# Kernel optimization log

Measured on AMD Instinct MI355X. Metric: run time of the kernel, lower is better.

## Reference

```python
import jax, jax.numpy as jnp
import numpy as np

B, S, H = 32, 2048, 1024
UNITS = 1024


def setup_inputs() -> dict:
    key = jax.random.key(0)
    ks = jax.random.split(key, 8)
    scale_h = 1.0 / np.sqrt(H)
    scale_u = 1.0 / np.sqrt(UNITS)
    return {
        "query": jax.random.normal(ks[0], (B, H), dtype=jnp.float32),
        "values": jax.random.normal(ks[1], (B, S, H), dtype=jnp.float32),
        "W1": jax.random.normal(ks[2], (H, UNITS), dtype=jnp.float32) * scale_h,
        "b1": jnp.zeros((UNITS,), dtype=jnp.float32),
        "W2": jax.random.normal(ks[3], (H, UNITS), dtype=jnp.float32) * scale_h,
        "b2": jnp.zeros((UNITS,), dtype=jnp.float32),
        "V": jax.random.normal(ks[4], (UNITS, 1), dtype=jnp.float32) * scale_u,
        "bv": jnp.zeros((1,), dtype=jnp.float32),
    }


def reference(query, values, W1, b1, W2, b2, V, bv):
    # proj_v: [B, S, units]; proj_q: [B, 1, units] (query expanded on time axis)
    proj_v = jnp.einsum("bsh,hu->bsu", values, W1) + b1
    proj_q = (query @ W2 + b2)[:, None, :]
    # score: [B, S, 1]
    score = jnp.tanh(proj_v + proj_q) @ V + bv
    attention_weights = jax.nn.softmax(score, axis=1)  # softmax over seq axis
    context_vector = jnp.sum(attention_weights * values, axis=1)  # [B, H]
    return context_vector, attention_weights
```

## Files before the change

### kernel.cpp

```cpp
#include <hip/hip_runtime.h>

#define H 1024
#define UNITS 1024
#define BATCH 32
#define SEQ 2048
#define M_TOT (BATCH * SEQ)

typedef __attribute__((ext_vector_type(8))) short bf16x8;
typedef __attribute__((ext_vector_type(8))) unsigned short u16x8;
typedef __attribute__((ext_vector_type(4))) float f32x4;

__device__ __forceinline__ unsigned short f2bf(float f) {
  union { float f; unsigned u; } x; x.f = f;
  unsigned r = x.u + 0x7FFFu + ((x.u >> 16) & 1u);
  return (unsigned short)(r >> 16);
}
__device__ __forceinline__ float bf2f(unsigned short h) {
  union { unsigned u; float f; } x; x.u = (unsigned)h << 16;
  return x.f;
}

__device__ __forceinline__ void gll16(const unsigned short* g, unsigned short* l) {
  __builtin_amdgcn_global_load_lds(
      (const __attribute__((address_space(1))) void*)g,
      (__attribute__((address_space(3))) void*)l, 16, 0, 0);
}

__global__ void k_cast(const float* __restrict__ in, unsigned short* __restrict__ out) {
  size_t i = ((size_t)blockIdx.x * 256 + threadIdx.x) * 8;
  float4 v0 = *reinterpret_cast<const float4*>(in + i);
  float4 v1 = *reinterpret_cast<const float4*>(in + i + 4);
  union { unsigned short h[8]; u16x8 v; } p;
  p.h[0] = f2bf(v0.x); p.h[1] = f2bf(v0.y); p.h[2] = f2bf(v0.z); p.h[3] = f2bf(v0.w);
  p.h[4] = f2bf(v1.x); p.h[5] = f2bf(v1.y); p.h[6] = f2bf(v1.z); p.h[7] = f2bf(v1.w);
  *reinterpret_cast<u16x8*>(out + i) = p.v;
}

__global__ void k_transpose_w1(const float* __restrict__ W1, unsigned short* __restrict__ W1T) {
  __shared__ float tile[32][33];
  int bx = blockIdx.x, by = blockIdx.y;
  int tx = threadIdx.x, ty = threadIdx.y;
#pragma unroll
  for (int i = 0; i < 4; ++i)
    tile[ty + i * 8][tx] = W1[(by * 32 + ty + i * 8) * UNITS + bx * 32 + tx];
  __syncthreads();
#pragma unroll
  for (int i = 0; i < 4; ++i)
    W1T[(bx * 32 + ty + i * 8) * H + by * 32 + tx] = f2bf(tile[tx][ty + i * 8]);
}

__global__ void k_projq(const float* __restrict__ query, const float* __restrict__ W2,
                        const float* __restrict__ b2, float* __restrict__ projq) {
  __shared__ float q[H];
  int b = blockIdx.x;
  int u = blockIdx.y * 256 + threadIdx.x;
  for (int i = threadIdx.x; i < H; i += 256) q[i] = query[b * H + i];
  __syncthreads();
  float acc = 0.f;
#pragma unroll 8
  for (int k = 0; k < H; ++k) acc = fmaf(q[k], W2[k * UNITS + u], acc);
  projq[b * UNITS + u] = acc + b2[u];
}

#define BM 256
#define BN 256
#define NT 16

__global__ __launch_bounds__(512, 2) void k_score3(
    const unsigned short* __restrict__ Vb,
    const unsigned short* __restrict__ W1T,
    const float* __restrict__ b1,
    const float* __restrict__ projq,
    const float* __restrict__ V,
    float* __restrict__ scores)
{
  __shared__ unsigned short As[2][256][64];
  __shared__ unsigned short Bs[2][256][64];

  const int tid = threadIdx.x;
  const int lane = tid & 63;
  const int wave = tid >> 6;
  const int wm = wave >> 2;
  const int wn = wave & 3;
  const int li = lane & 15, hi = lane >> 4;
  const int lx = li & 7;

  const int g = blockIdx.x;
  const int xcd = g & 7;
  const int local = g >> 3;
  const int n_t = local & 3;
  const int m_t = xcd + ((local >> 2) << 3);
  const int m0 = m_t * BM;
  const int n0 = n_t * BN;

  const int crow = lane >> 3;
  const int scol = ((lane & 7) ^ crow) << 3;

  auto STAGE_A = [&](int bf, int kt) {
#pragma unroll
    for (int q = 0; q < 4; ++q) {
      int r = wave * 32 + q * 8;
      gll16(&Vb[(size_t)(m0 + r + crow) * H + kt * 64 + scol], &As[bf][r][0]);
    }
  };
  auto STAGE_B = [&](int bf, int kt) {
#pragma unroll
    for (int q = 0; q < 4; ++q) {
      int r = wave * 32 + q * 8;
      gll16(&W1T[(size_t)(n0 + r + crow) * H + kt * 64 + scol], &Bs[bf][r][0]);
    }
  };

  f32x4 acc[8][4] = {};

  STAGE_A(0, 0);
  STAGE_B(0, 0);

#pragma unroll 2
  for (int c = 0; c < NT; ++c) {
    const int buf = c & 1, nbuf = buf ^ 1;
    const int cn = (c < NT - 1) ? c + 1 : NT - 1;

    asm volatile("s_waitcnt vmcnt(0)" ::: "memory");
    __builtin_amdgcn_s_barrier();

    bf16x8 a[8], b0, b1v;

    STAGE_A(nbuf, cn);
#pragma unroll
    for (int i = 0; i < 8; ++i)
      a[i] = *reinterpret_cast<const bf16x8*>(
          &As[buf][wm * 128 + i * 16 + li][(hi ^ lx) << 3]);
    b0  = *reinterpret_cast<const bf16x8*>(&Bs[buf][wn * 64 +  0 + li][(hi ^ lx) << 3]);
    b1v = *reinterpret_cast<const bf16x8*>(&Bs[buf][wn * 64 + 16 + li][(hi ^ lx) << 3]);
    __builtin_amdgcn_s_setprio(1);
#pragma unroll
    for (int i = 0; i < 8; ++i) {
      acc[i][0] = __builtin_amdgcn_mfma_f32_16x16x32_bf16(a[i], b0, acc[i][0], 0, 0, 0);
      acc[i][1] = __builtin_amdgcn_mfma_f32_16x16x32_bf16(a[i], b1v, acc[i][1], 0, 0, 0);
    }
    __builtin_amdgcn_s_setprio(0);

    STAGE_B(nbuf, cn);
    b0  = *reinterpret_cast<const bf16x8*>(&Bs[buf][wn * 64 + 32 + li][(hi ^ lx) << 3]);
    b1v = *reinterpret_cast<const bf16x8*>(&Bs[buf][wn * 64 + 48 + li][(hi ^ lx) << 3]);
    __builtin_amdgcn_s_setprio(1);
#pragma unroll
    for (int i = 0; i < 8; ++i) {
      acc[i][2] = __builtin_amdgcn_mfma_f32_16x16x32_bf16(a[i], b0, acc[i][2], 0, 0, 0);
      acc[i][3] = __builtin_amdgcn_mfma_f32_16x16x32_bf16(a[i], b1v, acc[i][3], 0, 0, 0);
    }
    __builtin_amdgcn_s_setprio(0);

#pragma unroll
    for (int i = 0; i < 8; ++i)
      a[i] = *reinterpret_cast<const bf16x8*>(
          &As[buf][wm * 128 + i * 16 + li][((4 + hi) ^ lx) << 3]);
    b0  = *reinterpret_cast<const bf16x8*>(&Bs[buf][wn * 64 +  0 + li][((4 + hi) ^ lx) << 3]);
    b1v = *reinterpret_cast<const bf16x8*>(&Bs[buf][wn * 64 + 16 + li][((4 + hi) ^ lx) << 3]);
    __builtin_amdgcn_s_setprio(1);
#pragma unroll
    for (int i = 0; i < 8; ++i) {
      acc[i][0] = __builtin_amdgcn_mfma_f32_16x16x32_bf16(a[i], b0, acc[i][0], 0, 0, 0);
      acc[i][1] = __builtin_amdgcn_mfma_f32_16x16x32_bf16(a[i], b1v, acc[i][1], 0, 0, 0);
    }
    __builtin_amdgcn_s_setprio(0);

    b0  = *reinterpret_cast<const bf16x8*>(&Bs[buf][wn * 64 + 32 + li][((4 + hi) ^ lx) << 3]);
    b1v = *reinterpret_cast<const bf16x8*>(&Bs[buf][wn * 64 + 48 + li][((4 + hi) ^ lx) << 3]);
    __builtin_amdgcn_s_setprio(1);
#pragma unroll
    for (int i = 0; i < 8; ++i) {
      acc[i][2] = __builtin_amdgcn_mfma_f32_16x16x32_bf16(a[i], b0, acc[i][2], 0, 0, 0);
      acc[i][3] = __builtin_amdgcn_mfma_f32_16x16x32_bf16(a[i], b1v, acc[i][3], 0, 0, 0);
    }
    __builtin_amdgcn_s_setprio(0);
  }

  const int b = m0 >> 11;
  float bias[4], vv[4];
#pragma unroll
  for (int j = 0; j < 4; ++j) {
    int u = n0 + wn * 64 + j * 16 + li;
    bias[j] = b1[u] + projq[b * UNITS + u];
    vv[j] = V[u];
  }
#pragma unroll
  for (int mi = 0; mi < 8; ++mi) {
#pragma unroll
    for (int r = 0; r < 4; ++r) {
      float s = 0.f;
#pragma unroll
      for (int j = 0; j < 4; ++j) {
        float x = acc[mi][j][r] + bias[j];
        float e = __expf(2.f * x);
        s += (1.f - 2.f / (e + 1.f)) * vv[j];
      }
      s += __shfl_xor(s, 1);
      s += __shfl_xor(s, 2);
      s += __shfl_xor(s, 4);
      s += __shfl_xor(s, 8);
      if (li == 0) {
        int row = m0 + wm * 128 + mi * 16 + hi * 4 + r;
        atomicAdd(&scores[row], s);
      }
    }
  }
}

#define FBM 128
#define FBN 128
#define FBK 64
#define LDK 72
__global__ __launch_bounds__(256) void k_score_f32(
    const float* __restrict__ values, const unsigned short* __restrict__ W1T,
    const float* __restrict__ b1, const float* __restrict__ projq,
    const float* __restrict__ V, float* __restrict__ scores)
{
  __shared__ unsigned short Asf[FBM][LDK];
  __shared__ unsigned short Bsf[FBN][LDK];
  const int tid = threadIdx.x;
  const int lane = tid & 63;
  const int wave = tid >> 6;
  const int wm = wave >> 1, wn = wave & 1;
  const int li = lane & 15, hi = lane >> 4;
  const int n0 = blockIdx.x * FBN;
  const int m0 = blockIdx.y * FBM;
  f32x4 acc[4][4] = {};
  for (int k0 = 0; k0 < H; k0 += FBK) {
    __syncthreads();
#pragma unroll
    for (int q = 0; q < 8; ++q) {
      int idx = q * 256 + tid;
      int row = idx >> 4;
      int kc = (idx & 15) << 2;
      float4 v = *reinterpret_cast<const float4*>(&values[(size_t)(m0 + row) * H + k0 + kc]);
      union { unsigned short h[4]; unsigned long long u64; } p;
      p.h[0] = f2bf(v.x); p.h[1] = f2bf(v.y); p.h[2] = f2bf(v.z); p.h[3] = f2bf(v.w);
      *reinterpret_cast<unsigned long long*>(&Asf[row][kc]) = p.u64;
    }
#pragma unroll
    for (int q = 0; q < 4; ++q) {
      int idx = q * 256 + tid;
      int row = idx >> 3;
      int kc = (idx & 7) << 3;
      *reinterpret_cast<u16x8*>(&Bsf[row][kc]) =
          *reinterpret_cast<const u16x8*>(&W1T[(size_t)(n0 + row) * H + k0 + kc]);
    }
    __syncthreads();
#pragma unroll
    for (int ks = 0; ks < 2; ++ks) {
      const int kofs = ks * 32 + 8 * hi;
      bf16x8 a[4], bb[4];
#pragma unroll
      for (int i = 0; i < 4; ++i)
        a[i] = *reinterpret_cast<const bf16x8*>(&Asf[wm * 64 + i * 16 + li][kofs]);
#pragma unroll
      for (int i = 0; i < 4; ++i)
        bb[i] = *reinterpret_cast<const bf16x8*>(&Bsf[wn * 64 + i * 16 + li][kofs]);
#pragma unroll
      for (int mi = 0; mi < 4; ++mi)
#pragma unroll
        for (int ni = 0; ni < 4; ++ni)
          acc[mi][ni] = __builtin_amdgcn_mfma_f32_16x16x32_bf16(a[mi], bb[ni], acc[mi][ni], 0, 0, 0);
    }
  }
  const int b = m0 >> 11;
  float bias[4], vv[4];
#pragma unroll
  for (int ni = 0; ni < 4; ++ni) {
    int u = n0 + wn * 64 + ni * 16 + li;
    bias[ni] = b1[u] + projq[b * UNITS + u];
    vv[ni] = V[u];
  }
#pragma unroll
  for (int mi = 0; mi < 4; ++mi) {
#pragma unroll
    for (int r = 0; r < 4; ++r) {
      float s = 0.f;
#pragma unroll
      for (int ni = 0; ni < 4; ++ni) {
        float x = acc[mi][ni][r] + bias[ni];
        float e = __expf(2.f * x);
        s += (1.f - 2.f / (e + 1.f)) * vv[ni];
      }
      s += __shfl_xor(s, 1);
      s += __shfl_xor(s, 2);
      s += __shfl_xor(s, 4);
      s += __shfl_xor(s, 8);
      if (li == 0) atomicAdd(&scores[m0 + wm * 64 + mi * 16 + hi * 4 + r], s);
    }
  }
}

__global__ void k_softmax(const float* __restrict__ scores, float* __restrict__ wts) {
  __shared__ float red[8];
  int b = blockIdx.x;
  int t = threadIdx.x;
  float v[8];
  float mx = -3.4e38f;
#pragma unroll
  for (int i = 0; i < 8; ++i) {
    v[i] = scores[b * SEQ + i * 256 + t];
    mx = fmaxf(mx, v[i]);
  }
#pragma unroll
  for (int o = 1; o < 64; o <<= 1) mx = fmaxf(mx, __shfl_xor(mx, o));
  if ((t & 63) == 0) red[t >> 6] = mx;
  __syncthreads();
  mx = fmaxf(fmaxf(red[0], red[1]), fmaxf(red[2], red[3]));
  float sum = 0.f;
#pragma unroll
  for (int i = 0; i < 8; ++i) { v[i] = __expf(v[i] - mx); sum += v[i]; }
#pragma unroll
  for (int o = 1; o < 64; o <<= 1) sum += __shfl_xor(sum, o);
  if ((t & 63) == 0) red[4 + (t >> 6)] = sum;
  __syncthreads();
  float inv = 1.f / (red[4] + red[5] + red[6] + red[7]);
#pragma unroll
  for (int i = 0; i < 8; ++i) wts[b * SEQ + i * 256 + t] = v[i] * inv;
}

__global__ void k_context_bf(const unsigned short* __restrict__ Vb,
                             const float* __restrict__ wts, float* __restrict__ ctx) {
  int b = blockIdx.x, sc = blockIdx.y;
  int h4 = threadIdx.x * 4;
  const unsigned short* vb = Vb + (size_t)b * SEQ * H;
  float a0 = 0, a1 = 0, a2 = 0, a3 = 0;
  int s0 = sc * 128;
#pragma unroll 4
  for (int s = s0; s < s0 + 128; ++s) {
    float w = wts[b * SEQ + s];
    ushort4 v = *reinterpret_cast<const ushort4*>(&vb[(size_t)s * H + h4]);
    a0 = fmaf(w, bf2f(v.x), a0);
    a1 = fmaf(w, bf2f(v.y), a1);
    a2 = fmaf(w, bf2f(v.z), a2);
    a3 = fmaf(w, bf2f(v.w), a3);
  }
  atomicAdd(&ctx[b * H + h4 + 0], a0);
  atomicAdd(&ctx[b * H + h4 + 1], a1);
  atomicAdd(&ctx[b * H + h4 + 2], a2);
  atomicAdd(&ctx[b * H + h4 + 3], a3);
}

__global__ void k_context(const float* __restrict__ values, const float* __restrict__ wts,
                          float* __restrict__ ctx) {
  int b = blockIdx.x, hc = blockIdx.y, sc = blockIdx.z;
  int h = hc * 256 + threadIdx.x;
  const float* vb = values + (size_t)b * SEQ * H;
  float acc = 0.f;
  int s0 = sc * 128;
#pragma unroll 4
  for (int s = s0; s < s0 + 128; ++s)
    acc = fmaf(wts[b * SEQ + s], vb[(size_t)s * H + h], acc);
  atomicAdd(&ctx[b * H + h], acc);
}

extern "C" void kernel_launch(void* const* d_in, const int* in_sizes, int n_in,
                              void* d_out, int out_size, void* d_ws, size_t ws_size,
                              hipStream_t stream) {
  (void)in_sizes; (void)n_in; (void)out_size;
  const float* query  = (const float*)d_in[0];
  const float* values = (const float*)d_in[1];
  const float* W1     = (const float*)d_in[2];
  const float* b1     = (const float*)d_in[3];
  const float* W2     = (const float*)d_in[4];
  const float* b2     = (const float*)d_in[5];
  const float* V      = (const float*)d_in[6];

  float* out = (float*)d_out;
  float* ctx = out;
  float* wts = out + BATCH * H;

  const size_t vb_bytes = (size_t)M_TOT * H * 2;
  const size_t need = vb_bytes + (2u << 20) + (256u << 10) + (128u << 10);

  if (ws_size >= need) {
    char* ws = (char*)d_ws;
    unsigned short* Vb  = (unsigned short*)ws;
    unsigned short* W1T = (unsigned short*)(ws + vb_bytes);
    float* scores = (float*)(ws + vb_bytes + (2u << 20));
    float* projq  = (float*)(ws + vb_bytes + (2u << 20) + (256u << 10));

    hipMemsetAsync(scores, 0, M_TOT * sizeof(float), stream);
    hipMemsetAsync(ctx, 0, BATCH * H * sizeof(float), stream);

    k_cast<<<(M_TOT * H / 8) / 256, 256, 0, stream>>>(values, Vb);
    k_transpose_w1<<<dim3(32, 32), dim3(32, 8), 0, stream>>>(W1, W1T);
    k_projq<<<dim3(32, 4), 256, 0, stream>>>(query, W2, b2, projq);
    k_score3<<<(M_TOT / BM) * (UNITS / BN), 512, 0, stream>>>(Vb, W1T, b1, projq, V, scores);
    k_softmax<<<BATCH, 256, 0, stream>>>(scores, wts);
    k_context_bf<<<dim3(BATCH, 16), 256, 0, stream>>>(Vb, wts, ctx);
  } else {
    char* ws = (char*)d_ws;
    unsigned short* W1T = (unsigned short*)ws;
    float* scores = (float*)(ws + (2u << 20));
    float* projq  = (float*)(ws + (2u << 20) + (256u << 10));

    hipMemsetAsync(scores, 0, M_TOT * sizeof(float), stream);
    hipMemsetAsync(ctx, 0, BATCH * H * sizeof(float), stream);

    k_transpose_w1<<<dim3(32, 32), dim3(32, 8), 0, stream>>>(W1, W1T);
    k_projq<<<dim3(32, 4), 256, 0, stream>>>(query, W2, b2, projq);
    k_score_f32<<<dim3(UNITS / FBN, M_TOT / FBM), 256, 0, stream>>>(values, W1T, b1, projq, V, scores);
    k_softmax<<<BATCH, 256, 0, stream>>>(scores, wts);
    k_context<<<dim3(BATCH, H / 256, 16), 256, 0, stream>>>(values, wts, ctx);
  }
}
```

Baseline: 341.1 us.

## Deepen GEMM K-pipeline to four stages with K=32 tiles and repacked LDS layout

Switches the score GEMM main loop from a 2-buffer K=64 pipeline to a 4-buffer K=32 pipeline. Three tiles are prefetched ahead, and the wait is relaxed to vmcnt(8) so global loads stay in flight across iterations. The LDS layout packs two 32-wide rows per 64-short line with a new XOR swizzle, and all LDS reads are issued before the next stage's async loads. The goal is to hide global-load latency better, at the cost of twice as many barriers per K and a new swizzle whose correctness and bank-conflict behaviour have to hold.

After: 328.2 us. -3.8%, faster.

```diff
diff --git a/kernel.cpp b/kernel.cpp
--- a/kernel.cpp
+++ b/kernel.cpp
@@ -64,7 +64,7 @@
 
 #define BM 256
 #define BN 256
-#define NT 16
+#define NKT 32
 
 __global__ __launch_bounds__(512, 2) void k_score3(
     const unsigned short* __restrict__ Vb,
@@ -74,8 +74,8 @@
     const float* __restrict__ V,
     float* __restrict__ scores)
 {
-  __shared__ unsigned short As[2][256][64];
-  __shared__ unsigned short Bs[2][256][64];
+  __shared__ unsigned short As[4][128][64];
+  __shared__ unsigned short Bs[4][128][64];
 
   const int tid = threadIdx.x;
   const int lane = tid & 63;
@@ -83,7 +83,8 @@
   const int wm = wave >> 2;
   const int wn = wave & 3;
   const int li = lane & 15, hi = lane >> 4;
-  const int lx = li & 7;
+  const int lr2 = li >> 1;
+  const int pcol = (((((li & 1) << 2) + hi) ^ lr2) & 7) << 3;
 
   const int g = blockIdx.x;
   const int xcd = g & 7;
@@ -93,87 +94,58 @@
   const int m0 = m_t * BM;
   const int n0 = n_t * BN;
 
-  const int crow = lane >> 3;
-  const int scol = ((lane & 7) ^ crow) << 3;
+  const int sL = (lane & 7) ^ (lane >> 3);
+  const int srow = 2 * (lane >> 3) + (sL >> 2);
+  const int scol = (sL & 3) << 3;
 
   auto STAGE_A = [&](int bf, int kt) {
 #pragma unroll
-    for (int q = 0; q < 4; ++q) {
-      int r = wave * 32 + q * 8;
-      gll16(&Vb[(size_t)(m0 + r + crow) * H + kt * 64 + scol], &As[bf][r][0]);
+    for (int q = 0; q < 2; ++q) {
+      int mb = wave * 32 + q * 16;
+      gll16(&Vb[(size_t)(m0 + mb + srow) * H + kt * 32 + scol],
+            &As[bf][wave * 16 + q * 8][0]);
     }
   };
   auto STAGE_B = [&](int bf, int kt) {
 #pragma unroll
-    for (int q = 0; q < 4; ++q) {
-      int r = wave * 32 + q * 8;
-      gll16(&W1T[(size_t)(n0 + r + crow) * H + kt * 64 + scol], &Bs[bf][r][0]);
+    for (int q = 0; q < 2; ++q) {
+      int mb = wave * 32 + q * 16;
+      gll16(&W1T[(size_t)(n0 + mb + srow) * H + kt * 32 + scol],
+            &Bs[bf][wave * 16 + q * 8][0]);
     }
   };
 
   f32x4 acc[8][4] = {};
 
-  STAGE_A(0, 0);
-  STAGE_B(0, 0);
-
-#pragma unroll 2
-  for (int c = 0; c < NT; ++c) {
-    const int buf = c & 1, nbuf = buf ^ 1;
-    const int cn = (c < NT - 1) ? c + 1 : NT - 1;
-
-    asm volatile("s_waitcnt vmcnt(0)" ::: "memory");
+  STAGE_A(0, 0); STAGE_B(0, 0);
+  STAGE_A(1, 1); STAGE_B(1, 1);
+  STAGE_A(2, 2); STAGE_B(2, 2);
+
+#pragma unroll 4
+  for (int c = 0; c < NKT; ++c) {
+    const int buf = c & 3;
+    const int nbuf = (c + 3) & 3;
+    const int cn = (c < NKT - 3) ? c + 3 : NKT - 1;
+
+    asm volatile("s_waitcnt vmcnt(8)" ::: "memory");
     __builtin_amdgcn_s_barrier();
 
-    bf16x8 a[8], b0, b1v;
-
+    bf16x8 a[8], b[4];
+#pragma unroll
+    for (int i = 0; i < 8; ++i)
+      a[i] = *reinterpret_cast<const bf16x8*>(&As[buf][wm * 64 + i * 8 + lr2][pcol]);
     STAGE_A(nbuf, cn);
 #pragma unroll
+    for (int j = 0; j < 4; ++j)
+      b[j] = *reinterpret_cast<const bf16x8*>(&Bs[buf][wn * 32 + j * 8 + lr2][pcol]);
+    STAGE_B(nbuf, cn);
+
+    __builtin_amdgcn_s_setprio(1);
+#pragma unroll
     for (int i = 0; i < 8; ++i)
-      a[i] = *reinterpret_cast<const bf16x8*>(
-          &As[buf][wm * 128 + i * 16 + li][(hi ^ lx) << 3]);
-    b0  = *reinterpret_cast<const bf16x8*>(&Bs[buf][wn * 64 +  0 + li][(hi ^ lx) << 3]);
-    b1v = *reinterpret_cast<const bf16x8*>(&Bs[buf][wn * 64 + 16 + li][(hi ^ lx) << 3]);
-    __builtin_amdgcn_s_setprio(1);
-#pragma unroll
-    for (int i = 0; i < 8; ++i) {
-      acc[i][0] = __builtin_amdgcn_mfma_f32_16x16x32_bf16(a[i], b0, acc[i][0], 0, 0, 0);
-      acc[i][1] = __builtin_amdgcn_mfma_f32_16x16x32_bf16(a[i], b1v, acc[i][1], 0, 0, 0);
-    }
-    __builtin_amdgcn_s_setprio(0);
-
-    STAGE_B(nbuf, cn);
-    b0  = *reinterpret_cast<const bf16x8*>(&Bs[buf][wn * 64 + 32 + li][(hi ^ lx) << 3]);
-    b1v = *reinterpret_cast<const bf16x8*>(&Bs[buf][wn * 64 + 48 + li][(hi ^ lx) << 3]);
-    __builtin_amdgcn_s_setprio(1);
-#pragma unroll
-    for (int i = 0; i < 8; ++i) {
-      acc[i][2] = __builtin_amdgcn_mfma_f32_16x16x32_bf16(a[i], b0, acc[i][2], 0, 0, 0);
-      acc[i][3] = __builtin_amdgcn_mfma_f32_16x16x32_bf16(a[i], b1v, acc[i][3], 0, 0, 0);
-    }
-    __builtin_amdgcn_s_setprio(0);
-
-#pragma unroll
-    for (int i = 0; i < 8; ++i)
-      a[i] = *reinterpret_cast<const bf16x8*>(
-          &As[buf][wm * 128 + i * 16 + li][((4 + hi) ^ lx) << 3]);
-    b0  = *reinterpret_cast<const bf16x8*>(&Bs[buf][wn * 64 +  0 + li][((4 + hi) ^ lx) << 3]);
-    b1v = *reinterpret_cast<const bf16x8*>(&Bs[buf][wn * 64 + 16 + li][((4 + hi) ^ lx) << 3]);
-    __builtin_amdgcn_s_setprio(1);
-#pragma unroll
-    for (int i = 0; i < 8; ++i) {
-      acc[i][0] = __builtin_amdgcn_mfma_f32_16x16x32_bf16(a[i], b0, acc[i][0], 0, 0, 0);
-      acc[i][1] = __builtin_amdgcn_mfma_f32_16x16x32_bf16(a[i], b1v, acc[i][1], 0, 0, 0);
-    }
-    __builtin_amdgcn_s_setprio(0);
-
-    b0  = *reinterpret_cast<const bf16x8*>(&Bs[buf][wn * 64 + 32 + li][((4 + hi) ^ lx) << 3]);
-    b1v = *reinterpret_cast<const bf16x8*>(&Bs[buf][wn * 64 + 48 + li][((4 + hi) ^ lx) << 3]);
-    __builtin_amdgcn_s_setprio(1);
-#pragma unroll
-    for (int i = 0; i < 8; ++i) {
-      acc[i][2] = __builtin_amdgcn_mfma_f32_16x16x32_bf16(a[i], b0, acc[i][2], 0, 0, 0);
-      acc[i][3] = __builtin_amdgcn_mfma_f32_16x16x32_bf16(a[i], b1v, acc[i][3], 0, 0, 0);
-    }
+#pragma unroll
+      for (int j = 0; j < 4; ++j)
+        acc[i][j] = __builtin_amdgcn_mfma_f32_16x16x32_bf16(a[i], b[j], acc[i][j], 0, 0, 0);
     __builtin_amdgcn_s_setprio(0);
   }
 
```
